# Performance work log

Measured on AMD Instinct MI355X. Metric: run time of the kernel, lower is better.

Reference implementation:

```python
import math
import jax, jax.numpy as jnp
import numpy as np

KV_SIZE = 960
EPS = 1e-5  # InstanceNorm2d default eps


def _instance_norm(x):
    # x: [B, H, C, K]; InstanceNorm2d(affine=False): normalize each (b,h) plane
    mu = x.mean(axis=(-2, -1), keepdims=True)
    var = x.var(axis=(-2, -1), keepdims=True)  # biased variance, matches torch
    return (x - mu) * jax.lax.rsqrt(var + EPS)


def _branch(emb, Wq, K, V, Wo):
    # emb: [B,N,C], Wq: [H,C,C], K/V: [B,H,N,KV], Wo: [C,C]
    Q = jnp.einsum('bnc,hdc->bhnd', emb, Wq)                       # per-head Linear
    scores = jnp.einsum('bhnc,bhnk->bhck', Q, K) / math.sqrt(KV_SIZE)
    probs = jax.nn.softmax(_instance_norm(scores), axis=-1)        # [B,H,C,KV]
    ctx = jnp.einsum('bhck,bhnk->bhcn', probs, V)                  # [B,H,C,N]
    ctx = ctx.mean(axis=1).transpose(0, 2, 1)                      # mean over heads -> [B,N,C]
    return ctx @ Wo.T                                              # out Linear (no bias)


def setup_inputs() -> dict:
    key = jax.random.key(0)
    ks = jax.random.split(key, 16)
    B, N, H = 8, 1024, 4
    C = [64, 128, 256, 512]
    d = {}
    for i, c in enumerate(C):
        d[f'emb{i+1}'] = jax.random.normal(ks[i], (B, N, c), dtype=jnp.float32)
    d['emb_all'] = jax.random.normal(ks[4], (B, N, KV_SIZE), dtype=jnp.float32)
    for i, c in enumerate(C):
        d[f'Wq{i+1}'] = jax.random.normal(ks[5 + i], (H, c, c), dtype=jnp.float32) * 0.02
    d['Wk'] = jax.random.normal(ks[9], (H, KV_SIZE, KV_SIZE), dtype=jnp.float32) * 0.02
    d['Wv'] = jax.random.normal(ks[10], (H, KV_SIZE, KV_SIZE), dtype=jnp.float32) * 0.02
    for i, c in enumerate(C):
        d[f'Wo{i+1}'] = jax.random.normal(ks[11 + i], (c, c), dtype=jnp.float32) * 0.02
    return d


def reference(emb1, emb2, emb3, emb4, emb_all,
              Wq1, Wq2, Wq3, Wq4, Wk, Wv,
              Wo1, Wo2, Wo3, Wo4):
    # shared K/V: per-head Linear over emb_all -> [B,H,N,KV]
    K = jnp.einsum('bnk,hjk->bhnj', emb_all, Wk)
    V = jnp.einsum('bnk,hjk->bhnj', emb_all, Wv)
    O1 = _branch(emb1, Wq1, K, V, Wo1)
    O2 = _branch(emb2, Wq2, K, V, Wo2)
    O3 = _branch(emb3, Wq3, K, V, Wo3)
    O4 = _branch(emb4, Wq4, K, V, Wo4)
    return (O1, O2, O3, O4)
```

## Files before the change

### kernel.cpp

```cpp
#include <hip/hip_runtime.h>
#include <stdint.h>

typedef unsigned short u16;
typedef short bf16x8 __attribute__((ext_vector_type(8)));
typedef float f32x4 __attribute__((ext_vector_type(4)));
typedef u16 u16x4 __attribute__((ext_vector_type(4)));

__device__ __forceinline__ u16 f2bf(float f) {
    unsigned u = __builtin_bit_cast(unsigned, f);
    unsigned r = (u + 0x7fffu + ((u >> 16) & 1u)) >> 16;
    return (u16)r;
}
__device__ __forceinline__ float bf2f(u16 h) {
    unsigned u = ((unsigned)h) << 16;
    return __builtin_bit_cast(float, u);
}

typedef const __attribute__((address_space(1))) unsigned int* gptr_t;
typedef __attribute__((address_space(3))) unsigned int* lptr_t;
__device__ __forceinline__ void gload16(const void* g, void* l) {
    __builtin_amdgcn_global_load_lds((gptr_t)(uintptr_t)g, (lptr_t)(uintptr_t)l, 16, 0, 0);
}

__device__ __constant__ int d_offs[4] = {0, 512, 768, 896};
__device__ __constant__ int d_cs[4] = {512, 256, 128, 64};

__global__ __launch_bounds__(256) void cast_bf16(const float4* __restrict__ in,
                                                 u16x4* __restrict__ out, int n4) {
    int i = blockIdx.x * 256 + threadIdx.x;
    if (i < n4) {
        float4 f = in[i];
        u16x4 o = {f2bf(f.x), f2bf(f.y), f2bf(f.z), f2bf(f.w)};
        out[i] = o;
    }
}

#define AREAD(P)                                                                   \
    bf16x8 areg[MFP][2];                                                           \
    _Pragma("unroll") for (int f = 0; f < MFP; f++)                                \
        _Pragma("unroll") for (int kb = 0; kb < 2; kb++) {                         \
            int rl = ((P)*MFP + f) * 16 + la;                                      \
            areg[f][kb] = *(const bf16x8*)&lds[ao + rl * 64 +                      \
                                               (((kb * 4 + lk4) ^ (rl & 7)) << 3)]; \
        }
#define CLUSTER(P)                                                                 \
    __builtin_amdgcn_s_barrier();                                                  \
    asm volatile("s_waitcnt lgkmcnt(0)" ::: "memory");                             \
    __builtin_amdgcn_sched_barrier(0);                                             \
    __builtin_amdgcn_s_setprio(1);                                                 \
    _Pragma("unroll") for (int f = 0; f < MFP; f++)                                \
        _Pragma("unroll") for (int ni = 0; ni < 4; ni++)                           \
            _Pragma("unroll") for (int kb = 0; kb < 2; kb++)                       \
                acc[(P)*MFP + f][ni] = __builtin_amdgcn_mfma_f32_16x16x32_bf16(    \
                    areg[f][kb], breg[ni][kb], acc[(P)*MFP + f][ni], 0, 0, 0);     \
    __builtin_amdgcn_s_setprio(0);

template <int BM>
__global__ __launch_bounds__(512, 2) void gemm_nt_8ph(
    const u16* __restrict__ A, long sAb, long sAh, int lda,
    const u16* __restrict__ B, long sBb, long sBh, int ldb,
    u16* __restrict__ C, long sCb, long sCh, int ldc,
    int M, int N, int K, int hdiv, float alpha) {
    constexpr int NA = BM / 128;
    constexpr int MFP = BM / 128;
    constexpr int WTM = BM / 2;
    constexpr int NMF = WTM / 16;
    constexpr int APART = WTM * 64;
    constexpr int BPART = 128 * 64;
    constexpr int BUFSZ = 2 * APART + 2 * BPART;
    __shared__ u16 lds[2 * BUFSZ];

    int gx = gridDim.x, gy = gridDim.y;
    int nwg = gx * gy * gridDim.z;
    int orig = blockIdx.x + gx * (blockIdx.y + gy * blockIdx.z);
    int q = nwg >> 3, r = nwg & 7;
    int xcd = orig & 7, seq = orig >> 3;
    int wg = (xcd < r ? xcd * (q + 1) : r * (q + 1) + (xcd - r) * q) + seq;
    int bx = wg % gx, tmpw = wg / gx;
    int by = tmpw % gy, bz = tmpw / gy;

    int bb = bz / hdiv, hh = bz - bb * hdiv;
    const u16* Ab = A + (size_t)bb * sAb + (size_t)hh * sAh;
    const u16* Bb = B + (size_t)bb * sBb + (size_t)hh * sBh;
    u16* Cb = C + (size_t)bb * sCb + (size_t)hh * sCh;
    int tm = by * BM, tn = bx * 256;
    int t = threadIdx.x, lane = t & 63, w = t >> 6;
    int wm = w >> 2, wn = w & 3;
    int la = lane & 15, lk4 = lane >> 4;

    const u16* pA0[NA];
    const u16* pA1[NA];
    const u16* pB0[2];
    const u16* pB1[2];
#pragma unroll
    for (int i = 0; i < NA; i++) {
        int seg = i * 512 + t;
        int col = (((seg & 7) ^ ((seg >> 3) & 7)) << 3);
        int r0 = tm + (seg >> 3);
        if (r0 > M - 1) r0 = M - 1;
        pA0[i] = Ab + (size_t)r0 * lda + col;
        int r1 = tm + WTM + (seg >> 3);
        if (r1 > M - 1) r1 = M - 1;
        pA1[i] = Ab + (size_t)r1 * lda + col;
    }
#pragma unroll
    for (int i = 0; i < 2; i++) {
        int seg = i * 512 + t;
        int col = (((seg & 7) ^ ((seg >> 3) & 7)) << 3);
        int r0 = tn + (seg >> 3);
        if (r0 > N - 1) r0 = N - 1;
        pB0[i] = Bb + (size_t)r0 * ldb + col;
        int r1 = tn + 128 + (seg >> 3);
        if (r1 > N - 1) r1 = N - 1;
        pB1[i] = Bb + (size_t)r1 * ldb + col;
    }

    auto AOF = [&](int buf, int h) { return buf * BUFSZ + h * APART; };
    auto BOF = [&](int buf, int h) { return buf * BUFSZ + 2 * APART + h * BPART; };
    auto stA0 = [&](int buf) {
#pragma unroll
        for (int i = 0; i < NA; i++) {
            gload16(pA0[i], &lds[AOF(buf, 0) + (i * 512 + t) * 8]);
            pA0[i] += 64;
        }
    };
    auto stA1 = [&](int buf) {
#pragma unroll
        for (int i = 0; i < NA; i++) {
            gload16(pA1[i], &lds[AOF(buf, 1) + (i * 512 + t) * 8]);
            pA1[i] += 64;
        }
    };
    auto stB0 = [&](int buf) {
#pragma unroll
        for (int i = 0; i < 2; i++) {
            gload16(pB0[i], &lds[BOF(buf, 0) + (i * 512 + t) * 8]);
            pB0[i] += 64;
        }
    };
    auto stB1 = [&](int buf) {
#pragma unroll
        for (int i = 0; i < 2; i++) {
            gload16(pB1[i], &lds[BOF(buf, 1) + (i * 512 + t) * 8]);
            pB1[i] += 64;
        }
    };

    int nt = K / 64;
    stB0(0);
    stB1(0);
    stA0(0);
    stA1(0);
    if (nt > 1) {
        stB0(1);
        stB1(1);
        asm volatile("s_waitcnt vmcnt(4)" ::: "memory");
    } else {
        asm volatile("s_waitcnt vmcnt(0)" ::: "memory");
    }
    __builtin_amdgcn_s_barrier();

    f32x4 acc[NMF][4] = {};
    bf16x8 breg[4][2];

    for (int k = 0; k < nt; ++k) {
        int buf = k & 1, nbuf = buf ^ 1;
        int ao = AOF(buf, wm), bo = BOF(buf, wn >> 1);
        int brow0 = (wn & 1) * 64;
        bool s1 = (k + 1 < nt), s2 = (k + 2 < nt);
        {
            AREAD(0)
#pragma unroll
            for (int ni = 0; ni < 4; ni++)
#pragma unroll
                for (int kb = 0; kb < 2; kb++) {
                    int rl = brow0 + ni * 16 + la;
                    breg[ni][kb] = *(const bf16x8*)&lds[bo + rl * 64 +
                                                        (((kb * 4 + lk4) ^ (rl & 7)) << 3)];
                }
            if (s1) stA0(nbuf);
            CLUSTER(0)
        }
        {
            AREAD(1)
            if (s1) stA1(nbuf);
            CLUSTER(1)
        }
        {
            AREAD(2)
            if (s2) stB0(buf);
            CLUSTER(2)
        }
        {
            AREAD(3)
            if (s2) stB1(buf);
            CLUSTER(3)
            if (s2)
                asm volatile("s_waitcnt vmcnt(4)" ::: "memory");
            else
                asm volatile("s_waitcnt vmcnt(0)" ::: "memory");
            __builtin_amdgcn_s_barrier();
        }
    }
#pragma unroll
    for (int mi = 0; mi < NMF; mi++)
#pragma unroll
        for (int ni = 0; ni < 4; ni++)
#pragma unroll
            for (int r_ = 0; r_ < 4; r_++) {
                int m = tm + wm * WTM + mi * 16 + ((lane >> 4) << 2) + r_;
                int n = tn + wn * 64 + ni * 16 + la;
                if (m < M && n < N)
                    Cb[(size_t)m * ldc + n] = f2bf(acc[mi][ni][r_] * alpha);
            }
}

template <typename OUT>
__global__ __launch_bounds__(256) void gemm_nt128(
    const u16* __restrict__ A, long sAb, long sAh, int lda,
    const u16* __restrict__ B, long sBb, long sBh, int ldb,
    OUT* __restrict__ C, long sCb, long sCh, int ldc,
    int M, int N, int K, int hdiv, float alpha) {
    __shared__ u16 sA[128 * 64];
    __shared__ u16 sB[128 * 64];
    int gx = gridDim.x, gy = gridDim.y;
    int nwg = gx * gy * gridDim.z;
    int orig = blockIdx.x + gx * (blockIdx.y + gy * blockIdx.z);
    int q = nwg >> 3, r = nwg & 7;
    int xcd = orig & 7, seq = orig >> 3;
    int wg = (xcd < r ? xcd * (q + 1) : r * (q + 1) + (xcd - r) * q) + seq;
    int bx = wg % gx, tmpw = wg / gx;
    int by = tmpw % gy, bz = tmpw / gy;

    int bb = bz / hdiv, hh = bz - bb * hdiv;
    const u16* Ab = A + (size_t)bb * sAb + (size_t)hh * sAh;
    const u16* Bb = B + (size_t)bb * sBb + (size_t)hh * sBh;
    OUT* Cb = C + (size_t)bb * sCb + (size_t)hh * sCh;
    int tm = by * 128, tn = bx * 128;
    int t = threadIdx.x, lane = t & 63, w = t >> 6;
    int wr = w >> 1, wc = w & 1;
    int r0 = t >> 3, c0 = (t & 7) * 8;
    const u16* gA[4];
    const u16* gB[4];
#pragma unroll
    for (int i = 0; i < 4; i++) {
        int ar = tm + i * 32 + r0;
        if (ar > M - 1) ar = M - 1;
        gA[i] = Ab + (size_t)ar * lda + c0;
    }
#pragma unroll
    for (int i = 0; i < 4; i++) {
        int br = tn + i * 32 + r0;
        if (br > N - 1) br = N - 1;
        gB[i] = Bb + (size_t)br * ldb + c0;
    }
    f32x4 acc[4][4] = {};
    int la = lane & 15, lk = (lane >> 4) * 8;
    for (int k0 = 0; k0 < K; k0 += 64) {
#pragma unroll
        for (int i = 0; i < 4; i++) {
            gload16(gA[i], &sA[(i * 256 + t) * 8]);
            gA[i] += 64;
        }
#pragma unroll
        for (int i = 0; i < 4; i++) {
            gload16(gB[i], &sB[(i * 256 + t) * 8]);
            gB[i] += 64;
        }
        __syncthreads();
#pragma unroll
        for (int kk = 0; kk < 64; kk += 32) {
            bf16x8 a[4], b[4];
#pragma unroll
            for (int mi = 0; mi < 4; mi++)
                a[mi] = *(const bf16x8*)&sA[(wr * 64 + mi * 16 + la) * 64 + kk + lk];
#pragma unroll
            for (int ni = 0; ni < 4; ni++)
                b[ni] = *(const bf16x8*)&sB[(wc * 64 + ni * 16 + la) * 64 + kk + lk];
#pragma unroll
            for (int mi = 0; mi < 4; mi++)
#pragma unroll
                for (int ni = 0; ni < 4; ni++)
                    acc[mi][ni] = __builtin_amdgcn_mfma_f32_16x16x32_bf16(
                        a[mi], b[ni], acc[mi][ni], 0, 0, 0);
        }
        __syncthreads();
    }
#pragma unroll
    for (int mi = 0; mi < 4; mi++)
#pragma unroll
        for (int ni = 0; ni < 4; ni++)
#pragma unroll
            for (int r_ = 0; r_ < 4; r_++) {
                int m = tm + wr * 64 + mi * 16 + (lane >> 4) * 4 + r_;
                int n = tn + wc * 64 + ni * 16 + la;
                if (m < M && n < N) {
                    float v = acc[mi][ni][r_] * alpha;
                    if constexpr (sizeof(OUT) == 4)
                        Cb[(size_t)m * ldc + n] = v;
                    else
                        Cb[(size_t)m * ldc + n] = f2bf(v);
                }
            }
}

__global__ __launch_bounds__(256) void in_stats1(const u16* __restrict__ sc,
                                                 double* __restrict__ part,
                                                 int G, int mode, int C) {
    int p = blockIdx.y, g = blockIdx.x, t = threadIdx.x;
    size_t base;
    int n8;
    if (mode) {
        int z = p >> 2, i = p & 3;
        base = (size_t)z * 921600 + (size_t)d_offs[i] * 960;
        n8 = d_cs[i] * 120;
    } else {
        base = (size_t)p * C * 960;
        n8 = C * 120;
    }
    const u16* x = sc + base;
    double s = 0.0, q = 0.0;
    for (int i = g * 256 + t; i < n8; i += G * 256) {
        u16x4 a = *(const u16x4*)&x[i * 8];
        u16x4 b = *(const u16x4*)&x[i * 8 + 4];
#pragma unroll
        for (int j = 0; j < 4; j++) {
            float fa = bf2f(a[j]), fb = bf2f(b[j]);
            s += (double)fa + (double)fb;
            q += (double)fa * fa + (double)fb * fb;
        }
    }
#pragma unroll
    for (int o = 32; o; o >>= 1) {
        s += __shfl_down(s, o);
        q += __shfl_down(q, o);
    }
    __shared__ double rs[4], rq[4];
    int w = t >> 6;
    if ((t & 63) == 0) {
        rs[w] = s;
        rq[w] = q;
    }
    __syncthreads();
    if (t == 0) {
        part[2 * ((size_t)p * G + g)] = rs[0] + rs[1] + rs[2] + rs[3];
        part[2 * ((size_t)p * G + g) + 1] = rq[0] + rq[1] + rq[2] + rq[3];
    }
}

__global__ __launch_bounds__(64) void in_stats2(const double* __restrict__ part,
                                                float* __restrict__ stats,
                                                int G, int mode, int C) {
    int p = blockIdx.x, t = threadIdx.x;
    int cnt = (mode ? d_cs[p & 3] : C) * 960;
    double s = 0.0, q = 0.0;
    if (t < G) {
        s = part[2 * ((size_t)p * G + t)];
        q = part[2 * ((size_t)p * G + t) + 1];
    }
#pragma unroll
    for (int o = 32; o; o >>= 1) {
        s += __shfl_down(s, o);
        q += __shfl_down(q, o);
    }
    if (t == 0) {
        float mu = (float)(s / cnt);
        float var = (float)(q / cnt) - mu * mu;
        stats[2 * p] = mu;
        stats[2 * p + 1] = rsqrtf(var + 1e-5f);
    }
}

__global__ __launch_bounds__(256) void norm_softmax_cat(const u16* __restrict__ sc,
                                                        const float* __restrict__ stats,
                                                        u16* __restrict__ prB) {
    int row = blockIdx.x;
    int z = row / 960, c = row - z * 960;
    int i = c < 512 ? 0 : (c < 768 ? 1 : (c < 896 ? 2 : 3));
    int plane = z * 4 + i;
    int b = z >> 2, h = z & 3;
    const u16* x = sc + (size_t)row * 960;
    u16* o = prB + (((size_t)b * 960 + c) * 4 + h) * 960;
    float mu = stats[2 * plane], rs = stats[2 * plane + 1];
    int t = threadIdx.x;
    bool act = t < 240;
    float v[4];
    float mx = -1e30f;
    if (act) {
        u16x4 d = *(const u16x4*)&x[t * 4];
#pragma unroll
        for (int j = 0; j < 4; j++) {
            v[j] = (bf2f(d[j]) - mu) * rs;
            mx = fmaxf(mx, v[j]);
        }
    }
    __shared__ float r1[4], r2[4];
#pragma unroll
    for (int o_ = 32; o_; o_ >>= 1) mx = fmaxf(mx, __shfl_xor(mx, o_));
    int w = t >> 6;
    if ((t & 63) == 0) r1[w] = mx;
    __syncthreads();
    mx = fmaxf(fmaxf(r1[0], r1[1]), fmaxf(r1[2], r1[3]));
    float s = 0.f;
    if (act) {
#pragma unroll
        for (int j = 0; j < 4; j++) {
            v[j] = __expf(v[j] - mx);
            s += v[j];
        }
    }
#pragma unroll
    for (int o_ = 32; o_; o_ >>= 1) s += __shfl_xor(s, o_);
    if ((t & 63) == 0) r2[w] = s;
    __syncthreads();
    s = r2[0] + r2[1] + r2[2] + r2[3];
    float inv = 1.0f / s;
    if (act) {
        u16x4 ov;
#pragma unroll
        for (int j = 0; j < 4; j++) ov[j] = f2bf(v[j] * inv);
        *(u16x4*)&o[t * 4] = ov;
    }
}

__global__ __launch_bounds__(256) void norm_softmax_ip(u16* sc,
                                                       const float* __restrict__ stats,
                                                       int C) {
    int row = blockIdx.x;
    int plane = row / C;
    u16* x = sc + (size_t)row * 960;
    float mu = stats[2 * plane], rs = stats[2 * plane + 1];
    int t = threadIdx.x;
    bool act = t < 240;
    float v[4];
    float mx = -1e30f;
    if (act) {
        u16x4 d = *(const u16x4*)&x[t * 4];
#pragma unroll
        for (int j = 0; j < 4; j++) {
            v[j] = (bf2f(d[j]) - mu) * rs;
            mx = fmaxf(mx, v[j]);
        }
    }
    __shared__ float r1[4], r2[4];
#pragma unroll
    for (int o = 32; o; o >>= 1) mx = fmaxf(mx, __shfl_xor(mx, o));
    int w = t >> 6;
    if ((t & 63) == 0) r1[w] = mx;
    __syncthreads();
    mx = fmaxf(fmaxf(r1[0], r1[1]), fmaxf(r1[2], r1[3]));
    float s = 0.f;
    if (act) {
#pragma unroll
        for (int j = 0; j < 4; j++) {
            v[j] = __expf(v[j] - mx);
            s += v[j];
        }
    }
#pragma unroll
    for (int o = 32; o; o >>= 1) s += __shfl_xor(s, o);
    if ((t & 63) == 0) r2[w] = s;
    __syncthreads();
    s = r2[0] + r2[1] + r2[2] + r2[3];
    float inv = 1.0f / s;
    if (act) {
        u16x4 o;
#pragma unroll
        for (int j = 0; j < 4; j++) o[j] = f2bf(v[j] * inv);
        *(u16x4*)&x[t * 4] = o;
    }
}

__global__ __launch_bounds__(256) void mean_heads(const u16* __restrict__ ctx, long ps,
                                                  u16* __restrict__ cm, int C) {
    int b = blockIdx.z;
    int n0 = blockIdx.x * 64, c0 = blockIdx.y * 64;
    __shared__ float sm[64][65];
    int t = threadIdx.x;
    float acc[16];
#pragma unroll
    for (int j = 0; j < 16; j++) acc[j] = 0.f;
    for (int h = 0; h < 4; h++) {
        const u16* p = ctx + (size_t)(b * 4 + h) * ps;
#pragma unroll
        for (int j = 0; j < 16; j++) {
            int lin = j * 256 + t;
            int cc = lin >> 6, nn = lin & 63;
            acc[j] += bf2f(p[(size_t)(c0 + cc) * 1024 + n0 + nn]);
        }
    }
#pragma unroll
    for (int j = 0; j < 16; j++) {
        int lin = j * 256 + t;
        sm[lin >> 6][lin & 63] = acc[j] * 0.25f;
    }
    __syncthreads();
#pragma unroll
    for (int j = 0; j < 16; j++) {
        int lin = j * 256 + t;
        int nn = lin >> 6, cc = lin & 63;
        cm[((size_t)b * 1024 + n0 + nn) * C + c0 + cc] = f2bf(sm[cc][nn]);
    }
}

extern "C" void kernel_launch(void* const* d_in, const int* in_sizes, int n_in,
                              void* d_out, int out_size, void* d_ws, size_t ws_size,
                              hipStream_t stream) {
    const int B = 8, NN = 1024, KV = 960;
    const int Cs[4] = {64, 128, 256, 512};
    const int ord[4] = {3, 2, 1, 0};
    const int offs[4] = {0, 512, 768, 896};
    const float* emb[4];
    for (int i = 0; i < 4; i++) emb[i] = (const float*)d_in[i];
    const float* embAll = (const float*)d_in[4];
    const float* Wq[4];
    for (int i = 0; i < 4; i++) Wq[i] = (const float*)d_in[5 + i];
    const float* Wk = (const float*)d_in[9];
    const float* Wv = (const float*)d_in[10];
    const float* Wo[4];
    for (int i = 0; i < 4; i++) Wo[i] = (const float*)d_in[11 + i];
    float* out = (float*)d_out;
    size_t outOff[4];
    {
        size_t o = 0;
        for (int i = 0; i < 4; i++) { outOff[i] = o; o += (size_t)B * NN * Cs[i]; }
    }

    const size_t SKV = 62914560;
    const size_t SSC = 58982400;
    const size_t SWQ = 2785280, SWO = 696320, SCM = 8388608;
    const size_t SPART = 131072, SST = 1024;
    const size_t SMALL = SWQ + SWO + SCM + SPART + SST;
    const size_t NEED_BAT = SSC + 3 * SKV + SMALL + 512;

    float invs = 1.0f / sqrtf((float)KV);
    auto g128 = [](int n) { return (n + 127) / 128; };

    if (ws_size >= NEED_BAT) {
        char* p = (char*)d_ws;
        u16* scB = (u16*)p;        p += SSC;
        u16* QtB = (u16*)p;        p += SKV;
        u16* Kt = (u16*)p;         p += SKV;
        u16* VbC = (u16*)p;        p += SKV;
        u16* wq[4];
        for (int i = 0; i < 4; i++) { wq[i] = (u16*)p; p += (size_t)4 * Cs[i] * Cs[i] * 2; }
        u16* wo[4];
        for (int i = 0; i < 4; i++) { wo[i] = (u16*)p; p += (size_t)Cs[i] * Cs[i] * 2; }
        u16* cmX = (u16*)p;        p += SCM;
        double* part = (double*)p; p += SPART;
        float* stats = (float*)p;

        u16* eA = scB;
        u16* wk = (u16*)((char*)scB + 15728640);
        u16* wv = (u16*)((char*)scB + 23101440);
        u16* prB = QtB;
        u16* cmC = scB;

        auto castL = [&](const float* s, u16* d, size_t n) {
            int n4 = (int)(n / 4);
            cast_bf16<<<(n4 + 255) / 256, 256, 0, stream>>>((const float4*)s, (u16x4*)d, n4);
        };
        castL(embAll, eA, (size_t)B * NN * KV);
        castL(Wk, wk, (size_t)4 * KV * KV);
        castL(Wv, wv, (size_t)4 * KV * KV);
        for (int i = 0; i < 4; i++) castL(Wq[i], wq[i], (size_t)4 * Cs[i] * Cs[i]);
        for (int i = 0; i < 4; i++) castL(Wo[i], wo[i], (size_t)Cs[i] * Cs[i]);

        gemm_nt_8ph<256><<<dim3(4, 4, 32), 512, 0, stream>>>(
            wk, 0, (long)KV * KV, KV, eA, (long)NN * KV, 0, KV,
            Kt, 4 * 983040L, 983040L, NN, KV, NN, KV, 4, 1.0f);
        gemm_nt_8ph<256><<<dim3(4, 4, 32), 512, 0, stream>>>(
            eA, (long)NN * KV, 0, KV, wv, 0, (long)KV * KV, KV,
            VbC, (long)NN * 3840, 960L, 3840, NN, KV, KV, 4, 1.0f);

        for (int j = 0; j < 4; j++) {
            int i = ord[j], C = Cs[i];
            castL(emb[i], cmX, (size_t)B * NN * C);
            if (C == 512) {
                gemm_nt_8ph<256><<<dim3(4, 2, 32), 512, 0, stream>>>(
                    wq[i], 0, (long)C * C, C, cmX, (long)NN * C, 0, C,
                    QtB + (size_t)offs[j] * 1024, 4 * 983040L, 983040L, NN,
                    C, NN, C, 4, 1.0f);
            } else {
                gemm_nt128<u16><<<dim3(8, g128(C), 32), 256, 0, stream>>>(
                    wq[i], 0, (long)C * C, C, cmX, (long)NN * C, 0, C,
                    QtB + (size_t)offs[j] * 1024, 4 * 983040L, 983040L, NN,
                    C, NN, C, 4, 1.0f);
            }
        }
        gemm_nt_8ph<256><<<dim3(4, 4, 32), 512, 0, stream>>>(
            QtB, 983040L, 0, NN, Kt, 983040L, 0, NN,
            scB, 921600L, 0, KV, 960, KV, NN, 1, invs);
        in_stats1<<<dim3(16, 128), 256, 0, stream>>>(scB, part, 16, 1, 0);
        in_stats2<<<128, 64, 0, stream>>>(part, stats, 16, 1, 0);
        norm_softmax_cat<<<32 * 960, 256, 0, stream>>>(scB, stats, prB);
        gemm_nt_8ph<128><<<dim3(4, 8, 8), 512, 0, stream>>>(
            VbC, (long)NN * 3840, 0, 3840, prB, (long)960 * 3840, 0, 3840,
            cmC, (long)NN * 960, 0, 960, NN, 960, 3840, 1, 0.25f);
        for (int j = 0; j < 4; j++) {
            int i = ord[j], C = Cs[i];
            gemm_nt128<float><<<dim3(g128(C), 8, 8), 256, 0, stream>>>(
                cmC + offs[j], (long)NN * 960, 0, 960, wo[i], 0, 0, C,
                out + outOff[i], (long)NN * C, 0, C, NN, C, C, 1, 1.0f);
        }
    } else {
        const size_t S1 = 33554432, S2 = 33554432;
        if (ws_size < S1 + S2 + 2 * SKV + SMALL + 512) return;
        char* p = (char*)d_ws;
        char* buf1 = p;            p += S1;
        char* buf2 = p;            p += S2;
        u16* Kt = (u16*)p;         p += SKV;
        u16* Vb = (u16*)p;         p += SKV;
        u16* wq[4];
        for (int i = 0; i < 4; i++) { wq[i] = (u16*)p; p += (size_t)4 * Cs[i] * Cs[i] * 2; }
        u16* wo[4];
        for (int i = 0; i < 4; i++) { wo[i] = (u16*)p; p += (size_t)Cs[i] * Cs[i] * 2; }
        u16* cmX = (u16*)p;        p += SCM;
        double* part = (double*)p; p += SPART;
        float* stats = (float*)p;

        u16* eA = (u16*)buf1;
        u16* wk = (u16*)(buf1 + 15728640);
        u16* wv = (u16*)(buf1 + 23101440);
        u16* sc = (u16*)buf1;
        u16* Qt = (u16*)buf2;
        u16* ctx = (u16*)buf2;

        auto castL = [&](const float* s, u16* d, size_t n) {
            int n4 = (int)(n / 4);
            cast_bf16<<<(n4 + 255) / 256, 256, 0, stream>>>((const float4*)s, (u16x4*)d, n4);
        };
        castL(embAll, eA, (size_t)B * NN * KV);
        castL(Wk, wk, (size_t)4 * KV * KV);
        castL(Wv, wv, (size_t)4 * KV * KV);
        for (int i = 0; i < 4; i++) castL(Wq[i], wq[i], (size_t)4 * Cs[i] * Cs[i]);
        for (int i = 0; i < 4; i++) castL(Wo[i], wo[i], (size_t)Cs[i] * Cs[i]);

        gemm_nt128<u16><<<dim3(8, 8, 32), 256, 0, stream>>>(
            wk, 0, (long)KV * KV, KV, eA, (long)NN * KV, 0, KV,
            Kt, 4 * 983040L, 983040L, NN, KV, NN, KV, 4, 1.0f);
        gemm_nt128<u16><<<dim3(8, 8, 32), 256, 0, stream>>>(
            eA, (long)NN * KV, 0, KV, wv, 0, (long)KV * KV, KV,
            Vb, 4 * 983040L, 983040L, KV, NN, KV, KV, 4, 1.0f);

        for (int i = 0; i < 4; i++) {
            int C = Cs[i];
            castL(emb[i], cmX, (size_t)B * NN * C);
            gemm_nt128<u16><<<dim3(8, g128(C), 32), 256, 0, stream>>>(
                wq[i], 0, (long)C * C, C, cmX, (long)NN * C, 0, C,
                Qt, 4L * C * NN, (long)C * NN, NN, C, NN, C, 4, 1.0f);
            gemm_nt128<u16><<<dim3(8, g128(C), 32), 256, 0, stream>>>(
                Qt, (long)C * NN, 0, NN, Kt, 983040L, 0, NN,
                sc, (long)C * KV, 0, KV, C, KV, NN, 1, invs);
            in_stats1<<<dim3(64, 32), 256, 0, stream>>>(sc, part, 64, 0, C);
            in_stats2<<<32, 64, 0, stream>>>(part, stats, 64, 0, C);
            norm_softmax_ip<<<32 * C, 256, 0, stream>>>(sc, stats, C);
            gemm_nt128<u16><<<dim3(8, g128(C), 32), 256, 0, stream>>>(
                sc, (long)C * KV, 0, KV, Vb, 983040L, 0, KV,
                ctx, (long)C * NN, 0, NN, C, NN, KV, 1, 1.0f);
            mean_heads<<<dim3(16, C / 64, B), 256, 0, stream>>>(
                ctx, (long)C * NN, cmX, C);
            gemm_nt128<float><<<dim3(g128(C), 8, B), 256, 0, stream>>>(
                cmX, (long)NN * C, 0, C, wo[i], 0, 0, C,
                out + outOff[i], (long)NN * C, 0, C, NN, C, C, 1, 1.0f);
        }
    }
}
```

Before: 459.9 us.

## Double-buffer A fragments in registers to overlap LDS reads with MFMA clusters

Restructures the 8-phase GEMM main loop so each phase reads the next A-fragment from LDS into an alternate register set while the MFMAs consume the previous one. Partial lgkmcnt waits replace full drains, and the first A fragment of the next k-tile is prefetched in the last phase. The vmcnt wait moves earlier and the prologue drops its nt>1 guard. The aim is to hide LDS read latency behind matrix math, at the cost of extra VGPRs and a prologue that assumes K covers at least two tiles.

```diff
diff --git a/kernel.cpp b/kernel.cpp
--- a/kernel.cpp
+++ b/kernel.cpp
@@ -35,25 +35,35 @@
     }
 }
 
-#define AREAD(P)                                                                   \
-    bf16x8 areg[MFP][2];                                                           \
+#define ARD(DST, BUFO, Q)                                                          \
     _Pragma("unroll") for (int f = 0; f < MFP; f++)                                \
         _Pragma("unroll") for (int kb = 0; kb < 2; kb++) {                         \
-            int rl = ((P)*MFP + f) * 16 + la;                                      \
-            areg[f][kb] = *(const bf16x8*)&lds[ao + rl * 64 +                      \
-                                               (((kb * 4 + lk4) ^ (rl & 7)) << 3)]; \
-        }
-#define CLUSTER(P)                                                                 \
-    __builtin_amdgcn_s_barrier();                                                  \
-    asm volatile("s_waitcnt lgkmcnt(0)" ::: "memory");                             \
+            int rl = ((Q)*MFP + f) * 16 + la;                                      \
+            DST[f][kb] = *(const bf16x8*)&lds[(BUFO) + rl * 64 +                   \
+                                              (((kb * 4 + lk4) ^ (rl & 7)) << 3)]; \
+        }
+#define BRD(BUFO)                                                                  \
+    _Pragma("unroll") for (int ni = 0; ni < 4; ni++)                               \
+        _Pragma("unroll") for (int kb = 0; kb < 2; kb++) {                         \
+            int rl = brow0 + ni * 16 + la;                                         \
+            breg[ni][kb] = *(const bf16x8*)&lds[(BUFO) + rl * 64 +                 \
+                                                (((kb * 4 + lk4) ^ (rl & 7)) << 3)]; \
+        }
+#define MMA(Q, SRC)                                                                \
     __builtin_amdgcn_sched_barrier(0);                                             \
     __builtin_amdgcn_s_setprio(1);                                                 \
     _Pragma("unroll") for (int f = 0; f < MFP; f++)                                \
         _Pragma("unroll") for (int ni = 0; ni < 4; ni++)                           \
             _Pragma("unroll") for (int kb = 0; kb < 2; kb++)                       \
-                acc[(P)*MFP + f][ni] = __builtin_amdgcn_mfma_f32_16x16x32_bf16(    \
-                    areg[f][kb], breg[ni][kb], acc[(P)*MFP + f][ni], 0, 0, 0);     \
+                acc[(Q)*MFP + f][ni] = __builtin_amdgcn_mfma_f32_16x16x32_bf16(    \
+                    SRC[f][kb], breg[ni][kb], acc[(Q)*MFP + f][ni], 0, 0, 0);      \
     __builtin_amdgcn_s_setprio(0);
+#define WAITL(N) asm volatile("s_waitcnt lgkmcnt(" #N ")" ::: "memory")
+#define WLGA               \
+    if constexpr (MFP == 2) \
+        WAITL(4);           \
+    else                    \
+        WAITL(2);
 
 template <int BM>
 __global__ __launch_bounds__(512, 2) void gemm_nt_8ph(
@@ -87,6 +97,7 @@
     int t = threadIdx.x, lane = t & 63, w = t >> 6;
     int wm = w >> 2, wn = w & 3;
     int la = lane & 15, lk4 = lane >> 4;
+    int brow0 = (wn & 1) * 64;
 
     const u16* pA0[NA];
     const u16* pA1[NA];
@@ -147,59 +158,60 @@
     };
 
     int nt = K / 64;
+    stA0(0);
+    stA1(0);
     stB0(0);
     stB1(0);
-    stA0(0);
-    stA1(0);
-    if (nt > 1) {
-        stB0(1);
-        stB1(1);
-        asm volatile("s_waitcnt vmcnt(4)" ::: "memory");
-    } else {
-        asm volatile("s_waitcnt vmcnt(0)" ::: "memory");
-    }
+    stB0(1);
+    stB1(1);
+    asm volatile("s_waitcnt vmcnt(4)" ::: "memory");
     __builtin_amdgcn_s_barrier();
 
     f32x4 acc[NMF][4] = {};
     bf16x8 breg[4][2];
+    bf16x8 aregA[MFP][2], aregB[MFP][2];
+    ARD(aregA, AOF(0, wm), 0)
 
     for (int k = 0; k < nt; ++k) {
         int buf = k & 1, nbuf = buf ^ 1;
-        int ao = AOF(buf, wm), bo = BOF(buf, wn >> 1);
-        int brow0 = (wn & 1) * 64;
+        int ao = AOF(buf, wm), bo = BOF(buf, wn >> 1), aoN = AOF(nbuf, wm);
         bool s1 = (k + 1 < nt), s2 = (k + 2 < nt);
         {
-            AREAD(0)
-#pragma unroll
-            for (int ni = 0; ni < 4; ni++)
-#pragma unroll
-                for (int kb = 0; kb < 2; kb++) {
-                    int rl = brow0 + ni * 16 + la;
-                    breg[ni][kb] = *(const bf16x8*)&lds[bo + rl * 64 +
-                                                        (((kb * 4 + lk4) ^ (rl & 7)) << 3)];
-                }
+            __builtin_amdgcn_s_barrier();
+            BRD(bo)
+            ARD(aregB, ao, 1)
             if (s1) stA0(nbuf);
-            CLUSTER(0)
+            WLGA
+            MMA(0, aregA)
         }
         {
-            AREAD(1)
+            __builtin_amdgcn_s_barrier();
+            ARD(aregA, ao, 2)
             if (s1) stA1(nbuf);
-            CLUSTER(1)
+            WLGA
+            MMA(1, aregB)
         }
         {
-            AREAD(2)
+            __builtin_amdgcn_s_barrier();
+            ARD(aregB, ao, 3)
             if (s2) stB0(buf);
-            CLUSTER(2)
-        }
-        {
-            AREAD(3)
-            if (s2) stB1(buf);
-            CLUSTER(3)
+            WLGA
+            MMA(2, aregA)
             if (s2)
-                asm volatile("s_waitcnt vmcnt(4)" ::: "memory");
+                asm volatile("s_waitcnt vmcnt(2)" ::: "memory");
             else
                 asm volatile("s_waitcnt vmcnt(0)" ::: "memory");
+        }
+        {
             __builtin_amdgcn_s_barrier();
+            if (s1) { ARD(aregA, aoN, 0) }
+            if (s2) stB1(buf);
+            if (s1) {
+                WLGA
+            } else {
+                WAITL(0);
+            }
+            MMA(3, aregB)
         }
     }
 #pragma unroll
```

Measured after the change: 472.6 us. 2.8% more time.
